# Optimization experiments

Measured on AMD Instinct MI355X. Metric: run time of the kernel, lower is better.

The kernel has to match this reference:

```python
import jax, jax.numpy as jnp
import numpy as np

TOPK = 5
LAMBDA_ALIGN_K = 16.0
MOM = 0.9          # EMA momentum
DEFAULT_SCORE = 0.5  # EMA bank default (bank starts empty)
EPS = 1e-8
NEG = 1.0e9


def pairwise_cosine(X):
    # torch F.normalize: X / max(||X||, eps)
    n = jnp.linalg.norm(X, axis=-1, keepdims=True)
    Xn = X / jnp.maximum(n, EPS)
    sim = Xn @ Xn.T
    return jnp.clip(sim, -1.0 + EPS, 1.0 - EPS)


def knn_mask(sim, allowed_base, topk=TOPK):
    B = sim.shape[0]
    eye = jnp.eye(B, dtype=sim.dtype)
    allowed = allowed_base * (1.0 - eye)
    masked = sim - NEG * eye
    masked = jnp.where(allowed < 0.5, -NEG, masked)
    masked = jnp.where(masked < 0.0, -NEG, masked)
    cand = (masked > 0).sum(axis=1)
    k = min(topk, max(B - 1, 1))
    keep_row = (cand >= topk).astype(sim.dtype)
    keep = keep_row[:, None] * keep_row[None, :]
    idx = jax.lax.top_k(masked, k)[1]                       # [B, k]
    M = jnp.zeros_like(sim).at[jnp.arange(B)[:, None], idx].set(1.0)
    M = jnp.maximum(M, M.T)
    return M * allowed * keep


def build_intra(sim, same, topk=TOPK):
    M = knn_mask(sim, same, topk)
    A = jnp.maximum(sim * M, 0.0) * same
    return A, M


def pga_loss(feats_sub, labels_sub):
    # feats_sub: [L, b, d]
    L = feats_sub.shape[0]
    same = (labels_sub[:, None] == labels_sub[None, :]).astype(jnp.float32)
    sims = jax.vmap(pairwise_cosine)(feats_sub)             # [L, b, b]
    A, M = jax.vmap(lambda s: build_intra(s, same))(sims)   # [L, b, b] each

    # EMA degree-based scores (no-grad in original; bank starts empty so
    # fetch-after-update == mom*default + (1-mom)*score_cur)
    S_intra = jnp.maximum(sims * same, 0.0)
    deg = jnp.maximum((S_intra > 0).sum(axis=2).astype(jnp.float32), 1.0)
    score_cur = jax.nn.sigmoid(S_intra.sum(axis=2) / deg)   # [L, b]
    ema = jax.lax.stop_gradient(MOM * DEFAULT_SCORE + (1.0 - MOM) * score_cur)

    # layer-pair masked MSE alignment, target detached
    A_deep = A[1:]
    A_tgt = jax.lax.stop_gradient(A[:-1])
    M_eff = jnp.maximum(M[:-1], M[1:])                      # [L-1, b, b]
    W = ema[:-1, :, None] * ema[:-1, None, :]               # [L-1, b, b]
    diff2 = (A_deep - A_tgt) ** 2 * W
    num = (diff2 * M_eff).sum(axis=(1, 2))
    den = jnp.maximum((M_eff * W).sum(axis=(1, 2)), EPS)
    terms = jnp.where(M_eff.sum(axis=(1, 2)) > 0, num / den, 0.0)
    raw = terms.sum() / max(L - 1, 1)
    return LAMBDA_ALIGN_K * raw


def setup_inputs() -> dict:
    key = jax.random.key(0)
    k1, k2 = jax.random.split(key)
    feats_final = jax.random.normal(k1, (8, 2048, 512), dtype=jnp.float32)
    labels = jax.random.randint(k2, (2048,), 0, 128).astype(jnp.int64)
    sample_ids = jnp.arange(2048, dtype=jnp.int64)
    return {"feats_final": feats_final, "labels": labels, "sample_ids": sample_ids}


def reference(feats_final, labels, sample_ids):
    # candidate subset from last layer (no-grad in original)
    X_last = feats_final[-1]
    S_last = pairwise_cosine(X_last)
    same_full = (labels[:, None] == labels[None, :]).astype(jnp.float32)
    _, M_last = build_intra(S_last, same_full)
    cand_mask = (M_last > 0).sum(axis=1) > 0
    idx_sub = jnp.nonzero(cand_mask)[0]  # eager (concrete) subselection
    feats_sub = feats_final[:, idx_sub]  # [L, b, d]
    labels_sub = labels[idx_sub]
    return pga_loss(feats_sub, labels_sub)
```

## Files before the change

kernel.cpp:

```cpp
#include <hip/hip_runtime.h>
#include <cmath>

#define NB   2048
#define ND   512
#define NL   8
#define NLAB 128
#define MAXM 64
#define TOPK_ 5
#define NTH  256
#define MAXSLOT 9
#define GSTRIDE (MAXM*MAXM)

#define SLOT_DECL(s) int off##s = -1; int lds##s = 0; float4 pre##s;
#define SLOT_INIT(s) { int idx = tid + (s)*NTH; if (idx < (m << 5)) { \
    int i = idx >> 5, k4 = idx & 31; \
    off##s = (g_s[i] << 9) + (k4 << 2); \
    lds##s = i * 132 + (k4 << 2); \
    pre##s = *(const float4*)(X + off##s); } }
#define SLOT_STORE(s) if (off##s >= 0) *(float4*)(XtF + lds##s) = pre##s;
#define SLOT_FETCH(s, kcn) if (off##s >= 0) pre##s = *(const float4*)(X + off##s + (kcn));

__global__ __launch_bounds__(NTH) void k_gram(
    const float* __restrict__ feats, const int* __restrict__ labels,
    float* __restrict__ G, int* __restrict__ cnt,
    unsigned long long* __restrict__ insub)
{
    __shared__ int wsum[4];
    __shared__ int g_s[MAXM];
    __shared__ float Xt[MAXM][132];
    __shared__ float rinvp[64];
    __shared__ unsigned long long tops_s[64];
    __shared__ unsigned char keep_s[64];
    float* XtF = &Xt[0][0];
    int c = blockIdx.x, l = blockIdx.y, tid = threadIdx.x;
    int lane = tid & 63, wv = tid >> 6;

    int my[8]; int n = 0; int base_i = tid * 8;
    for (int t = 0; t < 8; ++t) {
        int i = base_i + t;
        if (labels[i] == c) my[n++] = i;
    }
    int scan = n;
    #pragma unroll
    for (int off = 1; off < 64; off <<= 1) {
        int v = __shfl_up(scan, off);
        if (lane >= off) scan += v;
    }
    if (lane == 63) wsum[wv] = scan;
    __syncthreads();
    int w0 = wsum[0], w1 = wsum[1], w2 = wsum[2], w3 = wsum[3];
    int m = w0 + w1 + w2 + w3; if (m > MAXM) m = MAXM;
    int base = (wv > 0 ? w0 : 0) + (wv > 1 ? w1 : 0) + (wv > 2 ? w2 : 0);
    int excl = base + scan - n;
    for (int t = 0; t < n; ++t) {
        int slot = excl + t;
        if (slot < MAXM) g_s[slot] = my[t];
    }
    if (l == 0 && tid == 0) cnt[c] = m;
    __syncthreads();
    if (m == 0) {
        if (l == 7 && tid == 0) insub[c] = 0ull;
        return;
    }

    const float* X = feats + (size_t)l * NB * ND;

    SLOT_DECL(0) SLOT_DECL(1) SLOT_DECL(2) SLOT_DECL(3)
    SLOT_DECL(4) SLOT_DECL(5) SLOT_DECL(6) SLOT_DECL(7)
    SLOT_INIT(0) SLOT_INIT(1) SLOT_INIT(2) SLOT_INIT(3)
    SLOT_INIT(4) SLOT_INIT(5) SLOT_INIT(6) SLOT_INIT(7)

    const int P = m * (m + 1) / 2;
    float acc0[MAXSLOT], acc1[MAXSLOT];
    short is_[MAXSLOT], js_[MAXSLOT];
    int ns = 0;
    for (int p = tid; p < P; p += NTH) {
        int i = (int)((sqrtf(8.0f * (float)p + 1.0f) - 1.0f) * 0.5f);
        while (((i + 1) * (i + 2)) / 2 <= p) ++i;
        while ((i * (i + 1)) / 2 > p) --i;
        is_[ns] = (short)i;
        js_[ns] = (short)(p - (i * (i + 1)) / 2);
        acc0[ns] = 0.0f; acc1[ns] = 0.0f;
        ++ns;
    }

    for (int kc = 0; kc < ND; kc += 128) {
        if (kc) __syncthreads();
        SLOT_STORE(0) SLOT_STORE(1) SLOT_STORE(2) SLOT_STORE(3)
        SLOT_STORE(4) SLOT_STORE(5) SLOT_STORE(6) SLOT_STORE(7)
        __syncthreads();
        if (kc + 128 < ND) {
            int kcn = kc + 128;
            SLOT_FETCH(0, kcn) SLOT_FETCH(1, kcn) SLOT_FETCH(2, kcn) SLOT_FETCH(3, kcn)
            SLOT_FETCH(4, kcn) SLOT_FETCH(5, kcn) SLOT_FETCH(6, kcn) SLOT_FETCH(7, kcn)
        }
        for (int s = 0; s < ns; ++s) {
            int i = is_[s], j = js_[s];
            float a0 = acc0[s], a1 = acc1[s];
            #pragma unroll
            for (int k4 = 0; k4 < 32; ++k4) {
                float4 a = *(const float4*)&Xt[i][k4 << 2];
                float4 b = *(const float4*)&Xt[j][k4 << 2];
                a0 = fmaf(a.x, b.x, a0); a1 = fmaf(a.y, b.y, a1);
                a0 = fmaf(a.z, b.z, a0); a1 = fmaf(a.w, b.w, a1);
            }
            acc0[s] = a0; acc1[s] = a1;
        }
    }
    float* Gc = G + ((size_t)l * NLAB + c) * GSTRIDE;
    for (int s = 0; s < ns; ++s) {
        int i = is_[s], j = js_[s];
        float v = acc0[s] + acc1[s];
        Gc[i * MAXM + j] = v;
        Gc[j * MAXM + i] = v;
    }
    if (l != 7) return;

    float (*Gs)[65] = (float(*)[65])(&Xt[0][0]);
    __syncthreads();
    for (int s = 0; s < ns; ++s) {
        int i = is_[s], j = js_[s];
        float v = acc0[s] + acc1[s];
        Gs[i][j] = v; Gs[j][i] = v;
    }
    if (tid < m) for (int j = m; j < 64; ++j) Gs[tid][j] = -2.0f;
    __syncthreads();
    if (tid < 64) {
        rinvp[tid] = (tid < m) ? 1.0f / fmaxf(sqrtf(Gs[tid][tid]), 1e-8f) : 0.0f;
        keep_s[tid] = 0; tops_s[tid] = 0ull;
    }
    __syncthreads();
    unsigned long long tops = 0ull; bool keep = false;
    if (tid < m) {
        float ri = rinvp[tid];
        float v0=-1.f,v1=-1.f,v2=-1.f,v3=-1.f,v4=-1.f;
        int i0=0,i1=0,i2=0,i3=0,i4=0, cand=0;
        #pragma unroll 8
        for (int j = 0; j < 64; ++j) {
            float raw = Gs[tid][j];
            float v = fminf(fmaxf(raw * ri * rinvp[j], -1.0f), 1.0f);
            if (raw == -2.0f) v = -2.0f;
            if (v > 0.0f && j != tid) {
                ++cand;
                if      (v > v0) { v4=v3;i4=i3; v3=v2;i3=i2; v2=v1;i2=i1; v1=v0;i1=i0; v0=v;i0=j; }
                else if (v > v1) { v4=v3;i4=i3; v3=v2;i3=i2; v2=v1;i2=i1; v1=v;i1=j; }
                else if (v > v2) { v4=v3;i4=i3; v3=v2;i3=i2; v2=v;i2=j; }
                else if (v > v3) { v4=v3;i4=i3; v3=v;i3=j; }
                else if (v > v4) { v4=v;i4=j; }
            }
        }
        keep = (cand >= TOPK_);
        if (keep) tops = (1ull<<i0)|(1ull<<i1)|(1ull<<i2)|(1ull<<i3)|(1ull<<i4);
        keep_s[tid] = keep ? 1 : 0; tops_s[tid] = tops;
    }
    __syncthreads();
    unsigned long long Mrow = 0ull;
    if (tid < m && keep) {
        for (int j = 0; j < 64; ++j) {
            if (j == tid || !keep_s[j]) continue;
            if (((tops >> j) & 1ull) || ((tops_s[j] >> tid) & 1ull)) Mrow |= (1ull << j);
        }
    }
    if (tid < 64) {
        unsigned long long b = __ballot(Mrow != 0ull);
        if (tid == 0) insub[c] = b;
    }
}

__device__ __forceinline__ void load_tile(
    const float* __restrict__ Gc, int m, int tid, float (*Gs)[65], float* rinv)
{
    if (tid < 64) rinv[tid] = (tid < m) ? 1.0f / fmaxf(sqrtf(Gc[tid * MAXM + tid]), 1e-8f) : 0.0f;
    __syncthreads();
    int tot = m << 4;
    for (int idx4 = tid; idx4 < tot; idx4 += NTH) {
        int i = idx4 >> 4, j0 = (idx4 & 15) << 2;
        float4 raw = *(const float4*)(Gc + i * MAXM + j0);
        float ri = rinv[i];
        Gs[i][j0 + 0] = (j0 + 0 < m) ? fminf(fmaxf(raw.x * ri * rinv[j0 + 0], -1.0f), 1.0f) : -2.0f;
        Gs[i][j0 + 1] = (j0 + 1 < m) ? fminf(fmaxf(raw.y * ri * rinv[j0 + 1], -1.0f), 1.0f) : -2.0f;
        Gs[i][j0 + 2] = (j0 + 2 < m) ? fminf(fmaxf(raw.z * ri * rinv[j0 + 2], -1.0f), 1.0f) : -2.0f;
        Gs[i][j0 + 3] = (j0 + 3 < m) ? fminf(fmaxf(raw.w * ri * rinv[j0 + 3], -1.0f), 1.0f) : -2.0f;
    }
    __syncthreads();
}

__global__ __launch_bounds__(NTH) void k_decide(
    const float* __restrict__ G, const int* __restrict__ cnt,
    const unsigned long long* __restrict__ insub,
    unsigned long long* __restrict__ Mbits, float* __restrict__ ema)
{
    __shared__ float Gs[64][65];
    __shared__ float rinv[64];
    __shared__ unsigned long long tops_s[64];
    __shared__ unsigned char keep_s[64];
    int c = blockIdx.x, l = blockIdx.y, tid = threadIdx.x;
    int m = cnt[c]; if (m > MAXM) m = MAXM;
    if (m == 0) return;
    unsigned long long sub = insub[c];

    const float* Gc = G + ((size_t)l * NLAB + c) * GSTRIDE;
    load_tile(Gc, m, tid, Gs, rinv);
    if (tid < 64) { keep_s[tid] = 0; tops_s[tid] = 0ull; }
    __syncthreads();
    unsigned long long tops = 0ull; bool keep = false; bool act = false;
    float emaval = 0.0f;
    if (tid < m) {
        act = (sub >> tid) & 1ull;
        if (act) {
            float v0=-1.f,v1=-1.f,v2=-1.f,v3=-1.f,v4=-1.f;
            int i0=0,i1=0,i2=0,i3=0,i4=0, cand=0, dg=0;
            float rs = 0.0f;
            #pragma unroll 8
            for (int j = 0; j < 64; ++j) {
                float v = Gs[tid][j];
                if (!((sub >> j) & 1ull)) v = -2.0f;
                if (v > 0.0f) {
                    rs += v; ++dg;
                    if (j != tid) {
                        ++cand;
                        if      (v > v0) { v4=v3;i4=i3; v3=v2;i3=i2; v2=v1;i2=i1; v1=v0;i1=i0; v0=v;i0=j; }
                        else if (v > v1) { v4=v3;i4=i3; v3=v2;i3=i2; v2=v1;i2=i1; v1=v;i1=j; }
                        else if (v > v2) { v4=v3;i4=i3; v3=v2;i3=i2; v2=v;i2=j; }
                        else if (v > v3) { v4=v3;i4=i3; v3=v;i3=j; }
                        else if (v > v4) { v4=v;i4=j; }
                    }
                }
            }
            keep = (cand >= TOPK_);
            if (keep) tops = (1ull<<i0)|(1ull<<i1)|(1ull<<i2)|(1ull<<i3)|(1ull<<i4);
            float deg = (float)(dg > 0 ? dg : 1);
            float score = 1.0f / (1.0f + expf(-rs / deg));
            emaval = 0.45f + 0.1f * score;
        }
        keep_s[tid] = keep ? 1 : 0; tops_s[tid] = tops;
    }
    __syncthreads();
    if (tid < m) {
        unsigned long long Mrow = 0ull;
        if (keep) {
            for (int j = 0; j < 64; ++j) {
                if (j == tid || !keep_s[j]) continue;
                if (((tops >> j) & 1ull) || ((tops_s[j] >> tid) & 1ull)) Mrow |= (1ull << j);
            }
        }
        Mbits[((size_t)l * NLAB + c) * MAXM + tid] = Mrow;
        ema[((size_t)l * NLAB + c) * MAXM + tid] = emaval;
    }
}

__global__ __launch_bounds__(NTH) void k_pairs(
    const float* __restrict__ G, const int* __restrict__ cnt,
    const unsigned long long* __restrict__ Mbits, const float* __restrict__ ema,
    float* __restrict__ partial)
{
    __shared__ float r0[64], r1[64];
    __shared__ unsigned long long M0s[64], M1s[64];
    __shared__ float es[64];
    __shared__ float red[12];
    int c = blockIdx.x, p = blockIdx.y, tid = threadIdx.x;
    int m = cnt[c]; if (m > MAXM) m = MAXM;
    const float* G0 = G + ((size_t)p       * NLAB + c) * GSTRIDE;
    const float* G1 = G + ((size_t)(p + 1) * NLAB + c) * GSTRIDE;
    if (tid < m) {
        M0s[tid] = Mbits[((size_t)p * NLAB + c) * MAXM + tid];
        M1s[tid] = Mbits[((size_t)(p + 1) * NLAB + c) * MAXM + tid];
        es[tid]  = ema[((size_t)p * NLAB + c) * MAXM + tid];
        r0[tid]  = 1.0f / fmaxf(sqrtf(G0[tid * MAXM + tid]), 1e-8f);
        r1[tid]  = 1.0f / fmaxf(sqrtf(G1[tid * MAXM + tid]), 1e-8f);
    }
    __syncthreads();
    float fn = 0.0f, fd = 0.0f, fc = 0.0f;
    for (int idx = tid; idx < (m << 6); idx += NTH) {
        int i = idx >> 6, j = idx & 63;
        if (j >= m) continue;
        bool b0 = (M0s[i] >> j) & 1ull;
        bool b1 = (M1s[i] >> j) & 1ull;
        if (b0 | b1) {
            float v0 = b0 ? fminf(fmaxf(G0[idx] * r0[i] * r0[j], -1.0f), 1.0f) : 0.0f;
            float v1 = b1 ? fminf(fmaxf(G1[idx] * r1[i] * r1[j], -1.0f), 1.0f) : 0.0f;
            float w = es[i] * es[j];
            float d = v1 - v0;
            fn = fmaf(d * d, w, fn);
            fd += w;
            fc += 1.0f;
        }
    }
    for (int off = 32; off > 0; off >>= 1) {
        fn += __shfl_down(fn, off);
        fd += __shfl_down(fd, off);
        fc += __shfl_down(fc, off);
    }
    int w = tid >> 6;
    if ((tid & 63) == 0) { red[w * 3] = fn; red[w * 3 + 1] = fd; red[w * 3 + 2] = fc; }
    __syncthreads();
    if (tid == 0) {
        float* dst = partial + ((size_t)p * NLAB + c) * 4;
        dst[0] = red[0] + red[3] + red[6] + red[9];
        dst[1] = red[1] + red[4] + red[7] + red[10];
        dst[2] = red[2] + red[5] + red[8] + red[11];
    }
}

__global__ void k_final(const float* __restrict__ partial, float* __restrict__ out)
{
    int tid = threadIdx.x;
    float total = 0.0f;
    for (int p = 0; p < NL - 1; ++p) {
        float n = 0.0f, d = 0.0f, cc = 0.0f;
        for (int c = tid; c < NLAB; c += 64) {
            const float* src = partial + ((size_t)p * NLAB + c) * 4;
            n += src[0]; d += src[1]; cc += src[2];
        }
        for (int off = 32; off > 0; off >>= 1) {
            n += __shfl_down(n, off);
            d += __shfl_down(d, off);
            cc += __shfl_down(cc, off);
        }
        if (tid == 0 && cc > 0.0f) total += n / fmaxf(d, 1e-8f);
    }
    if (tid == 0) out[0] = 16.0f * total / 7.0f;
}

extern "C" void kernel_launch(void* const* d_in, const int* in_sizes, int n_in,
                              void* d_out, int out_size, void* d_ws, size_t ws_size,
                              hipStream_t stream) {
    const float* feats  = (const float*)d_in[0];
    const int*   labels = (const int*)d_in[1];
    char* w = (char*)d_ws;
    size_t gbytes = (size_t)NL * NLAB * GSTRIDE * 4;
    float*    G       = (float*)(w);
    float*    partial = (float*)(w + gbytes);
    int*      cnt     = (int*)(w + gbytes + 14336);
    unsigned long long* insub = (unsigned long long*)(w + gbytes + 14848);
    unsigned long long* Mbits = (unsigned long long*)(w + gbytes + 16384);
    float*    ema     = (float*)(w + gbytes + 16384 + 524288);
    float*    out     = (float*)d_out;

    k_gram  <<<dim3(NLAB, NL), NTH, 0, stream>>>(feats, labels, G, cnt, insub);
    k_decide<<<dim3(NLAB, NL), NTH, 0, stream>>>(G, cnt, insub, Mbits, ema);
    k_pairs <<<dim3(NLAB, NL - 1), NTH, 0, stream>>>(G, cnt, Mbits, ema, partial);
    k_final <<<1, 64, 0, stream>>>(partial, out);
}
```

Before: 131.6 us.

## Fuse gram, decision and pair kernels into one per-class block

Replaces the three-kernel pipeline (Gram, kNN decide, pair loss) with a single kernel, one block per label. Each block streams all eight layers' features through double-buffered LDS, computes each Gram tile with 2x2 register blocking, normalizes it in LDS and runs the top-k and EMA logic there. It then accumulates the layer-pair loss on the fly, so the global Gram, mask and EMA buffers and two launches go away. The trade-off is a grid of only 128 blocks that walk the layers in sequence, which may leave much of the GPU idle and expose memory latency.

```diff
diff --git a/kernel.cpp b/kernel.cpp
--- a/kernel.cpp
+++ b/kernel.cpp
@@ -8,31 +8,115 @@
 #define MAXM 64
 #define TOPK_ 5
 #define NTH  256
-#define MAXSLOT 9
-#define GSTRIDE (MAXM*MAXM)
+
 
 #define SLOT_DECL(s) int off##s = -1; int lds##s = 0; float4 pre##s;
-#define SLOT_INIT(s) { int idx = tid + (s)*NTH; if (idx < (m << 5)) { \
+#define SLOT_SETUP(s) { int idx = tid + (s)*NTH; if (idx < (m << 5)) { \
     int i = idx >> 5, k4 = idx & 31; \
     off##s = (g_s[i] << 9) + (k4 << 2); \
-    lds##s = i * 132 + (k4 << 2); \
-    pre##s = *(const float4*)(X + off##s); } }
-#define SLOT_STORE(s) if (off##s >= 0) *(float4*)(XtF + lds##s) = pre##s;
-#define SLOT_FETCH(s, kcn) if (off##s >= 0) pre##s = *(const float4*)(X + off##s + (kcn));
-
-__global__ __launch_bounds__(NTH) void k_gram(
+    lds##s = i * 132 + (k4 << 2); } }
+#define SLOT_FETCH(s, srcb) if (off##s >= 0) pre##s = *(const float4*)((srcb) + off##s);
+#define SLOT_STORE(s) if (off##s >= 0) *(float4*)(Xcur + lds##s) = pre##s;
+
+#define TDECL(s) short ti##s = -1, tj##s = 0; \
+    float q##s##00a=0.f,q##s##00b=0.f,q##s##01a=0.f,q##s##01b=0.f, \
+          q##s##10a=0.f,q##s##10b=0.f,q##s##11a=0.f,q##s##11b=0.f;
+
+#define TSETUP(s) { int p = tid + (s)*NTH; if (p < TP) { \
+    int i = (int)((sqrtf(8.0f * (float)p + 1.0f) - 1.0f) * 0.5f); \
+    while (((i + 1) * (i + 2)) / 2 <= p) ++i; \
+    while ((i * (i + 1)) / 2 > p) --i; \
+    ti##s = (short)i; tj##s = (short)(p - (i * (i + 1)) / 2); } }
+
+#define TCOMP(s) if (ti##s >= 0) { \
+    const float* ra = Xcur + ((int)ti##s << 1) * 132; \
+    const float* rb = Xcur + ((int)tj##s << 1) * 132; \
+    _Pragma("unroll") \
+    for (int k4 = 0; k4 < 32; ++k4) { \
+        float4 a0v = *(const float4*)(ra + (k4 << 2)); \
+        float4 a1v = *(const float4*)(ra + 132 + (k4 << 2)); \
+        float4 b0v = *(const float4*)(rb + (k4 << 2)); \
+        float4 b1v = *(const float4*)(rb + 132 + (k4 << 2)); \
+        q##s##00a = fmaf(a0v.x, b0v.x, q##s##00a); q##s##00b = fmaf(a0v.y, b0v.y, q##s##00b); \
+        q##s##00a = fmaf(a0v.z, b0v.z, q##s##00a); q##s##00b = fmaf(a0v.w, b0v.w, q##s##00b); \
+        q##s##01a = fmaf(a0v.x, b1v.x, q##s##01a); q##s##01b = fmaf(a0v.y, b1v.y, q##s##01b); \
+        q##s##01a = fmaf(a0v.z, b1v.z, q##s##01a); q##s##01b = fmaf(a0v.w, b1v.w, q##s##01b); \
+        q##s##10a = fmaf(a1v.x, b0v.x, q##s##10a); q##s##10b = fmaf(a1v.y, b0v.y, q##s##10b); \
+        q##s##10a = fmaf(a1v.z, b0v.z, q##s##10a); q##s##10b = fmaf(a1v.w, b0v.w, q##s##10b); \
+        q##s##11a = fmaf(a1v.x, b1v.x, q##s##11a); q##s##11b = fmaf(a1v.y, b1v.y, q##s##11b); \
+        q##s##11a = fmaf(a1v.z, b1v.z, q##s##11a); q##s##11b = fmaf(a1v.w, b1v.w, q##s##11b); \
+    } }
+
+#define TWB(s) if (ti##s >= 0) { \
+    int ib = (int)ti##s << 1, jb = (int)tj##s << 1; \
+    float v00 = q##s##00a + q##s##00b; \
+    float v01 = q##s##01a + q##s##01b; \
+    float v10 = q##s##10a + q##s##10b; \
+    float v11 = q##s##11a + q##s##11b; \
+    Gt[ib][jb] = v00; Gt[jb][ib] = v00; \
+    if (jb + 1 < m) { Gt[ib][jb+1] = v01; Gt[jb+1][ib] = v01; } \
+    if (ib + 1 < m) { Gt[ib+1][jb] = v10; Gt[jb][ib+1] = v10; } \
+    if (ib + 1 < m && jb + 1 < m) { Gt[ib+1][jb+1] = v11; Gt[jb+1][ib+1] = v11; } \
+    q##s##00a=0.f;q##s##00b=0.f;q##s##01a=0.f;q##s##01b=0.f; \
+    q##s##10a=0.f;q##s##10b=0.f;q##s##11a=0.f;q##s##11b=0.f; }
+
+__device__ __forceinline__ void pairs_acc(
+    int p, int c, int m, int tid,
+    const float (*gA)[65], const float (*gB)[65],
+    const unsigned long long* MbA, const unsigned long long* MbB,
+    const float* es, float* red, float* __restrict__ partial)
+{
+    float fn = 0.0f, fd = 0.0f, fc = 0.0f;
+    for (int idx = tid; idx < (m << 6); idx += NTH) {
+        int i = idx >> 6, j = idx & 63;
+        if (j >= m) continue;
+        bool b0 = (MbA[i] >> j) & 1ull;
+        bool b1 = (MbB[i] >> j) & 1ull;
+        if (b0 | b1) {
+            float v0 = b0 ? gA[i][j] : 0.0f;
+            float v1 = b1 ? gB[i][j] : 0.0f;
+            float w = es[i] * es[j];
+            float d = v1 - v0;
+            fn = fmaf(d * d, w, fn);
+            fd += w;
+            fc += 1.0f;
+        }
+    }
+    for (int off = 32; off > 0; off >>= 1) {
+        fn += __shfl_down(fn, off);
+        fd += __shfl_down(fd, off);
+        fc += __shfl_down(fc, off);
+    }
+    int wvx = tid >> 6;
+    if ((tid & 63) == 0) { red[wvx*3] = fn; red[wvx*3+1] = fd; red[wvx*3+2] = fc; }
+    __syncthreads();
+    if (tid == 0) {
+        float* dst = partial + ((size_t)p * NLAB + c) * 4;
+        dst[0] = red[0] + red[3] + red[6] + red[9];
+        dst[1] = red[1] + red[4] + red[7] + red[10];
+        dst[2] = red[2] + red[5] + red[8] + red[11];
+    }
+    __syncthreads();
+}
+
+__global__ __launch_bounds__(NTH) void k_fused(
     const float* __restrict__ feats, const int* __restrict__ labels,
-    float* __restrict__ G, int* __restrict__ cnt,
-    unsigned long long* __restrict__ insub)
+    float* __restrict__ partial)
 {
     __shared__ int wsum[4];
     __shared__ int g_s[MAXM];
-    __shared__ float Xt[MAXM][132];
-    __shared__ float rinvp[64];
+    __shared__ float Xt[2][MAXM][132];
+    __shared__ float g2[2][MAXM][65];
+    __shared__ float g7[MAXM][65];
+    __shared__ float rinv[64];
+    __shared__ unsigned long long Mb[NL][64];
+    __shared__ float emas[NL][64];
     __shared__ unsigned long long tops_s[64];
     __shared__ unsigned char keep_s[64];
-    float* XtF = &Xt[0][0];
-    int c = blockIdx.x, l = blockIdx.y, tid = threadIdx.x;
+    __shared__ unsigned long long sub_s;
+    __shared__ float red[12];
+
+    int c = blockIdx.x, tid = threadIdx.x;
     int lane = tid & 63, wv = tid >> 6;
 
     int my[8]; int n = 0; int base_i = tid * 8;
@@ -56,250 +140,167 @@
         int slot = excl + t;
         if (slot < MAXM) g_s[slot] = my[t];
     }
-    if (l == 0 && tid == 0) cnt[c] = m;
     __syncthreads();
     if (m == 0) {
-        if (l == 7 && tid == 0) insub[c] = 0ull;
+        if (tid == 0) {
+            for (int p = 0; p < NL - 1; ++p) {
+                float* dst = partial + ((size_t)p * NLAB + c) * 4;
+                dst[0] = 0.0f; dst[1] = 0.0f; dst[2] = 0.0f;
+            }
+        }
         return;
     }
 
-    const float* X = feats + (size_t)l * NB * ND;
+    const size_t LSTR = (size_t)NB * ND;
 
     SLOT_DECL(0) SLOT_DECL(1) SLOT_DECL(2) SLOT_DECL(3)
     SLOT_DECL(4) SLOT_DECL(5) SLOT_DECL(6) SLOT_DECL(7)
-    SLOT_INIT(0) SLOT_INIT(1) SLOT_INIT(2) SLOT_INIT(3)
-    SLOT_INIT(4) SLOT_INIT(5) SLOT_INIT(6) SLOT_INIT(7)
-
-    const int P = m * (m + 1) / 2;
-    float acc0[MAXSLOT], acc1[MAXSLOT];
-    short is_[MAXSLOT], js_[MAXSLOT];
-    int ns = 0;
-    for (int p = tid; p < P; p += NTH) {
-        int i = (int)((sqrtf(8.0f * (float)p + 1.0f) - 1.0f) * 0.5f);
-        while (((i + 1) * (i + 2)) / 2 <= p) ++i;
-        while ((i * (i + 1)) / 2 > p) --i;
-        is_[ns] = (short)i;
-        js_[ns] = (short)(p - (i * (i + 1)) / 2);
-        acc0[ns] = 0.0f; acc1[ns] = 0.0f;
-        ++ns;
-    }
-
-    for (int kc = 0; kc < ND; kc += 128) {
-        if (kc) __syncthreads();
+    SLOT_SETUP(0) SLOT_SETUP(1) SLOT_SETUP(2) SLOT_SETUP(3)
+    SLOT_SETUP(4) SLOT_SETUP(5) SLOT_SETUP(6) SLOT_SETUP(7)
+    {
+        const float* xb = feats + (size_t)7 * LSTR;
+        SLOT_FETCH(0, xb) SLOT_FETCH(1, xb) SLOT_FETCH(2, xb) SLOT_FETCH(3, xb)
+        SLOT_FETCH(4, xb) SLOT_FETCH(5, xb) SLOT_FETCH(6, xb) SLOT_FETCH(7, xb)
+    }
+
+    const int R = (m + 1) >> 1;
+    const int TP = R * (R + 1) / 2;
+    TDECL(0) TDECL(1) TDECL(2)
+    TSETUP(0) TSETUP(1) TSETUP(2)
+
+    for (int t = 0; t < 32; ++t) {
+        float* Xcur = &Xt[t & 1][0][0];
         SLOT_STORE(0) SLOT_STORE(1) SLOT_STORE(2) SLOT_STORE(3)
         SLOT_STORE(4) SLOT_STORE(5) SLOT_STORE(6) SLOT_STORE(7)
         __syncthreads();
-        if (kc + 128 < ND) {
-            int kcn = kc + 128;
-            SLOT_FETCH(0, kcn) SLOT_FETCH(1, kcn) SLOT_FETCH(2, kcn) SLOT_FETCH(3, kcn)
-            SLOT_FETCH(4, kcn) SLOT_FETCH(5, kcn) SLOT_FETCH(6, kcn) SLOT_FETCH(7, kcn)
-        }
-        for (int s = 0; s < ns; ++s) {
-            int i = is_[s], j = js_[s];
-            float a0 = acc0[s], a1 = acc1[s];
-            #pragma unroll
-            for (int k4 = 0; k4 < 32; ++k4) {
-                float4 a = *(const float4*)&Xt[i][k4 << 2];
-                float4 b = *(const float4*)&Xt[j][k4 << 2];
-                a0 = fmaf(a.x, b.x, a0); a1 = fmaf(a.y, b.y, a1);
-                a0 = fmaf(a.z, b.z, a0); a1 = fmaf(a.w, b.w, a1);
-            }
-            acc0[s] = a0; acc1[s] = a1;
-        }
-    }
-    float* Gc = G + ((size_t)l * NLAB + c) * GSTRIDE;
-    for (int s = 0; s < ns; ++s) {
-        int i = is_[s], j = js_[s];
-        float v = acc0[s] + acc1[s];
-        Gc[i * MAXM + j] = v;
-        Gc[j * MAXM + i] = v;
-    }
-    if (l != 7) return;
-
-    float (*Gs)[65] = (float(*)[65])(&Xt[0][0]);
-    __syncthreads();
-    for (int s = 0; s < ns; ++s) {
-        int i = is_[s], j = js_[s];
-        float v = acc0[s] + acc1[s];
-        Gs[i][j] = v; Gs[j][i] = v;
-    }
-    if (tid < m) for (int j = m; j < 64; ++j) Gs[tid][j] = -2.0f;
-    __syncthreads();
-    if (tid < 64) {
-        rinvp[tid] = (tid < m) ? 1.0f / fmaxf(sqrtf(Gs[tid][tid]), 1e-8f) : 0.0f;
-        keep_s[tid] = 0; tops_s[tid] = 0ull;
-    }
-    __syncthreads();
-    unsigned long long tops = 0ull; bool keep = false;
-    if (tid < m) {
-        float ri = rinvp[tid];
-        float v0=-1.f,v1=-1.f,v2=-1.f,v3=-1.f,v4=-1.f;
-        int i0=0,i1=0,i2=0,i3=0,i4=0, cand=0;
-        #pragma unroll 8
-        for (int j = 0; j < 64; ++j) {
-            float raw = Gs[tid][j];
-            float v = fminf(fmaxf(raw * ri * rinvp[j], -1.0f), 1.0f);
-            if (raw == -2.0f) v = -2.0f;
-            if (v > 0.0f && j != tid) {
-                ++cand;
-                if      (v > v0) { v4=v3;i4=i3; v3=v2;i3=i2; v2=v1;i2=i1; v1=v0;i1=i0; v0=v;i0=j; }
-                else if (v > v1) { v4=v3;i4=i3; v3=v2;i3=i2; v2=v1;i2=i1; v1=v;i1=j; }
-                else if (v > v2) { v4=v3;i4=i3; v3=v2;i3=i2; v2=v;i2=j; }
-                else if (v > v3) { v4=v3;i4=i3; v3=v;i3=j; }
-                else if (v > v4) { v4=v;i4=j; }
-            }
-        }
-        keep = (cand >= TOPK_);
-        if (keep) tops = (1ull<<i0)|(1ull<<i1)|(1ull<<i2)|(1ull<<i3)|(1ull<<i4);
-        keep_s[tid] = keep ? 1 : 0; tops_s[tid] = tops;
-    }
-    __syncthreads();
-    unsigned long long Mrow = 0ull;
-    if (tid < m && keep) {
-        for (int j = 0; j < 64; ++j) {
-            if (j == tid || !keep_s[j]) continue;
-            if (((tops >> j) & 1ull) || ((tops_s[j] >> tid) & 1ull)) Mrow |= (1ull << j);
-        }
-    }
-    if (tid < 64) {
-        unsigned long long b = __ballot(Mrow != 0ull);
-        if (tid == 0) insub[c] = b;
-    }
-}
-
-__device__ __forceinline__ void load_tile(
-    const float* __restrict__ Gc, int m, int tid, float (*Gs)[65], float* rinv)
-{
-    if (tid < 64) rinv[tid] = (tid < m) ? 1.0f / fmaxf(sqrtf(Gc[tid * MAXM + tid]), 1e-8f) : 0.0f;
-    __syncthreads();
-    int tot = m << 4;
-    for (int idx4 = tid; idx4 < tot; idx4 += NTH) {
-        int i = idx4 >> 4, j0 = (idx4 & 15) << 2;
-        float4 raw = *(const float4*)(Gc + i * MAXM + j0);
-        float ri = rinv[i];
-        Gs[i][j0 + 0] = (j0 + 0 < m) ? fminf(fmaxf(raw.x * ri * rinv[j0 + 0], -1.0f), 1.0f) : -2.0f;
-        Gs[i][j0 + 1] = (j0 + 1 < m) ? fminf(fmaxf(raw.y * ri * rinv[j0 + 1], -1.0f), 1.0f) : -2.0f;
-        Gs[i][j0 + 2] = (j0 + 2 < m) ? fminf(fmaxf(raw.z * ri * rinv[j0 + 2], -1.0f), 1.0f) : -2.0f;
-        Gs[i][j0 + 3] = (j0 + 3 < m) ? fminf(fmaxf(raw.w * ri * rinv[j0 + 3], -1.0f), 1.0f) : -2.0f;
-    }
-    __syncthreads();
-}
-
-__global__ __launch_bounds__(NTH) void k_decide(
-    const float* __restrict__ G, const int* __restrict__ cnt,
-    const unsigned long long* __restrict__ insub,
-    unsigned long long* __restrict__ Mbits, float* __restrict__ ema)
-{
-    __shared__ float Gs[64][65];
-    __shared__ float rinv[64];
-    __shared__ unsigned long long tops_s[64];
-    __shared__ unsigned char keep_s[64];
-    int c = blockIdx.x, l = blockIdx.y, tid = threadIdx.x;
-    int m = cnt[c]; if (m > MAXM) m = MAXM;
-    if (m == 0) return;
-    unsigned long long sub = insub[c];
-
-    const float* Gc = G + ((size_t)l * NLAB + c) * GSTRIDE;
-    load_tile(Gc, m, tid, Gs, rinv);
-    if (tid < 64) { keep_s[tid] = 0; tops_s[tid] = 0ull; }
-    __syncthreads();
-    unsigned long long tops = 0ull; bool keep = false; bool act = false;
-    float emaval = 0.0f;
-    if (tid < m) {
-        act = (sub >> tid) & 1ull;
-        if (act) {
-            float v0=-1.f,v1=-1.f,v2=-1.f,v3=-1.f,v4=-1.f;
-            int i0=0,i1=0,i2=0,i3=0,i4=0, cand=0, dg=0;
-            float rs = 0.0f;
-            #pragma unroll 8
-            for (int j = 0; j < 64; ++j) {
-                float v = Gs[tid][j];
-                if (!((sub >> j) & 1ull)) v = -2.0f;
-                if (v > 0.0f) {
-                    rs += v; ++dg;
-                    if (j != tid) {
-                        ++cand;
-                        if      (v > v0) { v4=v3;i4=i3; v3=v2;i3=i2; v2=v1;i2=i1; v1=v0;i1=i0; v0=v;i0=j; }
-                        else if (v > v1) { v4=v3;i4=i3; v3=v2;i3=i2; v2=v1;i2=i1; v1=v;i1=j; }
-                        else if (v > v2) { v4=v3;i4=i3; v3=v2;i3=i2; v2=v;i2=j; }
-                        else if (v > v3) { v4=v3;i4=i3; v3=v;i3=j; }
-                        else if (v > v4) { v4=v;i4=j; }
+        if (t < 31) {
+            int tn = t + 1;
+            int Ln = ((tn >> 2) == 0) ? 7 : (tn >> 2) - 1;
+            const float* xb = feats + (size_t)Ln * LSTR + ((tn & 3) << 7);
+            SLOT_FETCH(0, xb) SLOT_FETCH(1, xb) SLOT_FETCH(2, xb) SLOT_FETCH(3, xb)
+            SLOT_FETCH(4, xb) SLOT_FETCH(5, xb) SLOT_FETCH(6, xb) SLOT_FETCH(7, xb)
+        }
+        TCOMP(0) TCOMP(1) TCOMP(2)
+
+        if ((t & 3) == 3) {
+            int sl = t >> 2;
+            int L = (sl == 0) ? 7 : sl - 1;
+            float (*Gt)[65] = (sl == 0) ? g7 : g2[L & 1];
+
+            TWB(0) TWB(1) TWB(2)
+            __syncthreads();
+            if (tid < 64) rinv[tid] = (tid < m) ? 1.0f / fmaxf(sqrtf(Gt[tid][tid]), 1e-8f) : 0.0f;
+            __syncthreads();
+            for (int idx = tid; idx < (m << 6); idx += NTH) {
+                int i = idx >> 6, j = idx & 63;
+                float x = -2.0f;
+                if (j < m) {
+                    float raw = Gt[i][j];
+                    x = fminf(fmaxf(raw * rinv[i] * rinv[j], -1.0f), 1.0f);
+                }
+                Gt[i][j] = x;
+            }
+            __syncthreads();
+
+            if (sl == 0) {
+                if (tid < 64) { keep_s[tid] = 0; tops_s[tid] = 0ull; }
+                __syncthreads();
+                unsigned long long tops = 0ull; bool keep = false;
+                if (tid < m) {
+                    float v0=-1.f,v1=-1.f,v2=-1.f,v3=-1.f,v4=-1.f;
+                    int i0=0,i1=0,i2=0,i3=0,i4=0, cand=0;
+                    #pragma unroll 8
+                    for (int j = 0; j < 64; ++j) {
+                        float v = g7[tid][j];
+                        if (v > 0.0f && j != tid) {
+                            ++cand;
+                            if      (v > v0) { v4=v3;i4=i3; v3=v2;i3=i2; v2=v1;i2=i1; v1=v0;i1=i0; v0=v;i0=j; }
+                            else if (v > v1) { v4=v3;i4=i3; v3=v2;i3=i2; v2=v1;i2=i1; v1=v;i1=j; }
+                            else if (v > v2) { v4=v3;i4=i3; v3=v2;i3=i2; v2=v;i2=j; }
+                            else if (v > v3) { v4=v3;i4=i3; v3=v;i3=j; }
+                            else if (v > v4) { v4=v;i4=j; }
+                        }
                     }
-                }
-            }
-            keep = (cand >= TOPK_);
-            if (keep) tops = (1ull<<i0)|(1ull<<i1)|(1ull<<i2)|(1ull<<i3)|(1ull<<i4);
-            float deg = (float)(dg > 0 ? dg : 1);
-            float score = 1.0f / (1.0f + expf(-rs / deg));
-            emaval = 0.45f + 0.1f * score;
-        }
-        keep_s[tid] = keep ? 1 : 0; tops_s[tid] = tops;
-    }
-    __syncthreads();
-    if (tid < m) {
-        unsigned long long Mrow = 0ull;
-        if (keep) {
-            for (int j = 0; j < 64; ++j) {
-                if (j == tid || !keep_s[j]) continue;
-                if (((tops >> j) & 1ull) || ((tops_s[j] >> tid) & 1ull)) Mrow |= (1ull << j);
-            }
-        }
-        Mbits[((size_t)l * NLAB + c) * MAXM + tid] = Mrow;
-        ema[((size_t)l * NLAB + c) * MAXM + tid] = emaval;
-    }
-}
-
-__global__ __launch_bounds__(NTH) void k_pairs(
-    const float* __restrict__ G, const int* __restrict__ cnt,
-    const unsigned long long* __restrict__ Mbits, const float* __restrict__ ema,
-    float* __restrict__ partial)
-{
-    __shared__ float r0[64], r1[64];
-    __shared__ unsigned long long M0s[64], M1s[64];
-    __shared__ float es[64];
-    __shared__ float red[12];
-    int c = blockIdx.x, p = blockIdx.y, tid = threadIdx.x;
-    int m = cnt[c]; if (m > MAXM) m = MAXM;
-    const float* G0 = G + ((size_t)p       * NLAB + c) * GSTRIDE;
-    const float* G1 = G + ((size_t)(p + 1) * NLAB + c) * GSTRIDE;
-    if (tid < m) {
-        M0s[tid] = Mbits[((size_t)p * NLAB + c) * MAXM + tid];
-        M1s[tid] = Mbits[((size_t)(p + 1) * NLAB + c) * MAXM + tid];
-        es[tid]  = ema[((size_t)p * NLAB + c) * MAXM + tid];
-        r0[tid]  = 1.0f / fmaxf(sqrtf(G0[tid * MAXM + tid]), 1e-8f);
-        r1[tid]  = 1.0f / fmaxf(sqrtf(G1[tid * MAXM + tid]), 1e-8f);
-    }
-    __syncthreads();
-    float fn = 0.0f, fd = 0.0f, fc = 0.0f;
-    for (int idx = tid; idx < (m << 6); idx += NTH) {
-        int i = idx >> 6, j = idx & 63;
-        if (j >= m) continue;
-        bool b0 = (M0s[i] >> j) & 1ull;
-        bool b1 = (M1s[i] >> j) & 1ull;
-        if (b0 | b1) {
-            float v0 = b0 ? fminf(fmaxf(G0[idx] * r0[i] * r0[j], -1.0f), 1.0f) : 0.0f;
-            float v1 = b1 ? fminf(fmaxf(G1[idx] * r1[i] * r1[j], -1.0f), 1.0f) : 0.0f;
-            float w = es[i] * es[j];
-            float d = v1 - v0;
-            fn = fmaf(d * d, w, fn);
-            fd += w;
-            fc += 1.0f;
-        }
-    }
-    for (int off = 32; off > 0; off >>= 1) {
-        fn += __shfl_down(fn, off);
-        fd += __shfl_down(fd, off);
-        fc += __shfl_down(fc, off);
-    }
-    int w = tid >> 6;
-    if ((tid & 63) == 0) { red[w * 3] = fn; red[w * 3 + 1] = fd; red[w * 3 + 2] = fc; }
-    __syncthreads();
-    if (tid == 0) {
-        float* dst = partial + ((size_t)p * NLAB + c) * 4;
-        dst[0] = red[0] + red[3] + red[6] + red[9];
-        dst[1] = red[1] + red[4] + red[7] + red[10];
-        dst[2] = red[2] + red[5] + red[8] + red[11];
-    }
+                    keep = (cand >= TOPK_);
+                    if (keep) tops = (1ull<<i0)|(1ull<<i1)|(1ull<<i2)|(1ull<<i3)|(1ull<<i4);
+                    keep_s[tid] = keep ? 1 : 0; tops_s[tid] = tops;
+                }
+                __syncthreads();
+                unsigned long long Mrow = 0ull;
+                if (tid < m && keep) {
+                    for (int j = 0; j < 64; ++j) {
+                        if (j == tid || !keep_s[j]) continue;
+                        if (((tops >> j) & 1ull) || ((tops_s[j] >> tid) & 1ull)) Mrow |= (1ull << j);
+                    }
+                }
+                if (tid < 64) {
+                    unsigned long long b = __ballot(Mrow != 0ull);
+                    if (tid == 0) sub_s = b;
+                }
+                __syncthreads();
+            }
+
+            if (tid < 64) { keep_s[tid] = 0; tops_s[tid] = 0ull; }
+            __syncthreads();
+            {
+                unsigned long long sub = sub_s;
+                unsigned long long tops = 0ull; bool keep = false; float emaval = 0.0f;
+                if (tid < m) {
+                    bool act = (sub >> tid) & 1ull;
+                    if (act) {
+                        float v0=-1.f,v1=-1.f,v2=-1.f,v3=-1.f,v4=-1.f;
+                        int i0=0,i1=0,i2=0,i3=0,i4=0, cand=0, dg=0;
+                        float rs = 0.0f;
+                        #pragma unroll 8
+                        for (int j = 0; j < 64; ++j) {
+                            float v = Gt[tid][j];
+                            if (!((sub >> j) & 1ull)) v = -2.0f;
+                            if (v > 0.0f) {
+                                rs += v; ++dg;
+                                if (j != tid) {
+                                    ++cand;
+                                    if      (v > v0) { v4=v3;i4=i3; v3=v2;i3=i2; v2=v1;i2=i1; v1=v0;i1=i0; v0=v;i0=j; }
+                                    else if (v > v1) { v4=v3;i4=i3; v3=v2;i3=i2; v2=v1;i2=i1; v1=v;i1=j; }
+                                    else if (v > v2) { v4=v3;i4=i3; v3=v2;i3=i2; v2=v;i2=j; }
+                                    else if (v > v3) { v4=v3;i4=i3; v3=v;i3=j; }
+                                    else if (v > v4) { v4=v;i4=j; }
+                                }
+                            }
+                        }
+                        keep = (cand >= TOPK_);
+                        if (keep) tops = (1ull<<i0)|(1ull<<i1)|(1ull<<i2)|(1ull<<i3)|(1ull<<i4);
+                        float deg = (float)(dg > 0 ? dg : 1);
+                        float score = 1.0f / (1.0f + expf(-rs / deg));
+                        emaval = 0.45f + 0.1f * score;
+                    }
+                    keep_s[tid] = keep ? 1 : 0; tops_s[tid] = tops;
+                }
+                __syncthreads();
+                if (tid < m) {
+                    unsigned long long Mrow = 0ull;
+                    if (keep) {
+                        for (int j = 0; j < 64; ++j) {
+                            if (j == tid || !keep_s[j]) continue;
+                            if (((tops >> j) & 1ull) || ((tops_s[j] >> tid) & 1ull)) Mrow |= (1ull << j);
+                        }
+                    }
+                    Mb[L][tid] = Mrow;
+                    emas[L][tid] = emaval;
+                }
+                __syncthreads();
+            }
+
+            if (sl >= 2) {
+                pairs_acc(L - 1, c, m, tid,
+                          (const float (*)[65])g2[(L - 1) & 1],
+                          (const float (*)[65])g2[L & 1],
+                          Mb[L - 1], Mb[L], emas[L - 1], red, partial);
+            }
+        }
+    }
+    pairs_acc(6, c, m, tid,
+              (const float (*)[65])g2[0], (const float (*)[65])g7,
+              Mb[6], Mb[7], emas[6], red, partial);
 }
 
 __global__ void k_final(const float* __restrict__ partial, float* __restrict__ out)
@@ -327,18 +328,9 @@
                               hipStream_t stream) {
     const float* feats  = (const float*)d_in[0];
     const int*   labels = (const int*)d_in[1];
-    char* w = (char*)d_ws;
-    size_t gbytes = (size_t)NL * NLAB * GSTRIDE * 4;
-    float*    G       = (float*)(w);
-    float*    partial = (float*)(w + gbytes);
-    int*      cnt     = (int*)(w + gbytes + 14336);
-    unsigned long long* insub = (unsigned long long*)(w + gbytes + 14848);
-    unsigned long long* Mbits = (unsigned long long*)(w + gbytes + 16384);
-    float*    ema     = (float*)(w + gbytes + 16384 + 524288);
-    float*    out     = (float*)d_out;
-
-    k_gram  <<<dim3(NLAB, NL), NTH, 0, stream>>>(feats, labels, G, cnt, insub);
-    k_decide<<<dim3(NLAB, NL), NTH, 0, stream>>>(G, cnt, insub, Mbits, ema);
-    k_pairs <<<dim3(NLAB, NL - 1), NTH, 0, stream>>>(G, cnt, Mbits, ema, partial);
-    k_final <<<1, 64, 0, stream>>>(partial, out);
+    float* partial = (float*)d_ws;
+    float* out     = (float*)d_out;
+
+    k_fused<<<dim3(NLAB), NTH, 0, stream>>>(feats, labels, partial);
+    k_final<<<1, 64, 0, stream>>>(partial, out);
 }
```

Measured after the change: 268.3 us. +103.9%, slower.

## Fuse decide and pair kernels; store normalized cosine tiles from gram kernel

Applied to the files above, without the earlier changes.

The gram kernel now normalizes each class Gram tile into cosines in shared memory and writes the normalized tile to global memory with float4 stores. The separate decide and pairs kernels are merged into one kernel per layer pair. It loads both layers' tiles into LDS, computes kNN masks and EMA weights for each with two wavefronts, then reduces the masked MSE. This drops one launch and the Mbits/ema global round trip. The cost is that the kNN and EMA work for interior layers is done twice, and the fused kernel uses more shared memory.

```diff
diff --git a/kernel.cpp b/kernel.cpp
--- a/kernel.cpp
+++ b/kernel.cpp
@@ -107,14 +107,6 @@
             acc0[s] = a0; acc1[s] = a1;
         }
     }
-    float* Gc = G + ((size_t)l * NLAB + c) * GSTRIDE;
-    for (int s = 0; s < ns; ++s) {
-        int i = is_[s], j = js_[s];
-        float v = acc0[s] + acc1[s];
-        Gc[i * MAXM + j] = v;
-        Gc[j * MAXM + i] = v;
-    }
-    if (l != 7) return;
 
     float (*Gs)[65] = (float(*)[65])(&Xt[0][0]);
     __syncthreads();
@@ -125,21 +117,32 @@
     }
     if (tid < m) for (int j = m; j < 64; ++j) Gs[tid][j] = -2.0f;
     __syncthreads();
-    if (tid < 64) {
-        rinvp[tid] = (tid < m) ? 1.0f / fmaxf(sqrtf(Gs[tid][tid]), 1e-8f) : 0.0f;
-        keep_s[tid] = 0; tops_s[tid] = 0ull;
-    }
+    if (tid < 64) rinvp[tid] = (tid < m) ? 1.0f / fmaxf(sqrtf(Gs[tid][tid]), 1e-8f) : 0.0f;
+    __syncthreads();
+    for (int idx = tid; idx < (m << 6); idx += NTH) {
+        int i = idx >> 6, j = idx & 63;
+        if (j < m) {
+            float raw = Gs[i][j];
+            Gs[i][j] = fminf(fmaxf(raw * rinvp[i] * rinvp[j], -1.0f), 1.0f);
+        }
+    }
+    __syncthreads();
+    float* Gc = G + ((size_t)l * NLAB + c) * GSTRIDE;
+    for (int idx4 = tid; idx4 < (m << 4); idx4 += NTH) {
+        int i = idx4 >> 4, j0 = (idx4 & 15) << 2;
+        *(float4*)(Gc + i * MAXM + j0) = *(const float4*)&Gs[i][j0];
+    }
+    if (l != 7) return;
+
+    if (tid < 64) { keep_s[tid] = 0; tops_s[tid] = 0ull; }
     __syncthreads();
     unsigned long long tops = 0ull; bool keep = false;
     if (tid < m) {
-        float ri = rinvp[tid];
         float v0=-1.f,v1=-1.f,v2=-1.f,v3=-1.f,v4=-1.f;
         int i0=0,i1=0,i2=0,i3=0,i4=0, cand=0;
         #pragma unroll 8
         for (int j = 0; j < 64; ++j) {
-            float raw = Gs[tid][j];
-            float v = fminf(fmaxf(raw * ri * rinvp[j], -1.0f), 1.0f);
-            if (raw == -2.0f) v = -2.0f;
+            float v = Gs[tid][j];
             if (v > 0.0f && j != tid) {
                 ++cand;
                 if      (v > v0) { v4=v3;i4=i3; v3=v2;i3=i2; v2=v1;i2=i1; v1=v0;i1=i0; v0=v;i0=j; }
@@ -167,57 +170,50 @@
     }
 }
 
-__device__ __forceinline__ void load_tile(
-    const float* __restrict__ Gc, int m, int tid, float (*Gs)[65], float* rinv)
-{
-    if (tid < 64) rinv[tid] = (tid < m) ? 1.0f / fmaxf(sqrtf(Gc[tid * MAXM + tid]), 1e-8f) : 0.0f;
-    __syncthreads();
-    int tot = m << 4;
-    for (int idx4 = tid; idx4 < tot; idx4 += NTH) {
-        int i = idx4 >> 4, j0 = (idx4 & 15) << 2;
-        float4 raw = *(const float4*)(Gc + i * MAXM + j0);
-        float ri = rinv[i];
-        Gs[i][j0 + 0] = (j0 + 0 < m) ? fminf(fmaxf(raw.x * ri * rinv[j0 + 0], -1.0f), 1.0f) : -2.0f;
-        Gs[i][j0 + 1] = (j0 + 1 < m) ? fminf(fmaxf(raw.y * ri * rinv[j0 + 1], -1.0f), 1.0f) : -2.0f;
-        Gs[i][j0 + 2] = (j0 + 2 < m) ? fminf(fmaxf(raw.z * ri * rinv[j0 + 2], -1.0f), 1.0f) : -2.0f;
-        Gs[i][j0 + 3] = (j0 + 3 < m) ? fminf(fmaxf(raw.w * ri * rinv[j0 + 3], -1.0f), 1.0f) : -2.0f;
-    }
-    __syncthreads();
-}
-
-__global__ __launch_bounds__(NTH) void k_decide(
+__global__ __launch_bounds__(NTH) void k_pairdec(
     const float* __restrict__ G, const int* __restrict__ cnt,
     const unsigned long long* __restrict__ insub,
-    unsigned long long* __restrict__ Mbits, float* __restrict__ ema)
+    float* __restrict__ partial)
 {
-    __shared__ float Gs[64][65];
-    __shared__ float rinv[64];
-    __shared__ unsigned long long tops_s[64];
-    __shared__ unsigned char keep_s[64];
-    int c = blockIdx.x, l = blockIdx.y, tid = threadIdx.x;
+    __shared__ float Gs0[64][65];
+    __shared__ float Gs1[64][65];
+    __shared__ unsigned long long tops0[64], tops1[64];
+    __shared__ unsigned char keep0[64], keep1[64];
+    __shared__ unsigned long long M0s[64], M1s[64];
+    __shared__ float es[64];
+    __shared__ float red[12];
+    int c = blockIdx.x, p = blockIdx.y, tid = threadIdx.x;
+    int lane = tid & 63, wv = tid >> 6;
     int m = cnt[c]; if (m > MAXM) m = MAXM;
-    if (m == 0) return;
     unsigned long long sub = insub[c];
 
-    const float* Gc = G + ((size_t)l * NLAB + c) * GSTRIDE;
-    load_tile(Gc, m, tid, Gs, rinv);
-    if (tid < 64) { keep_s[tid] = 0; tops_s[tid] = 0ull; }
-    __syncthreads();
-    unsigned long long tops = 0ull; bool keep = false; bool act = false;
-    float emaval = 0.0f;
-    if (tid < m) {
-        act = (sub >> tid) & 1ull;
+    const float* G0 = G + ((size_t)p       * NLAB + c) * GSTRIDE;
+    const float* G1 = G + ((size_t)(p + 1) * NLAB + c) * GSTRIDE;
+    for (int idx4 = tid; idx4 < (m << 4); idx4 += NTH) {
+        int i = idx4 >> 4, j0 = (idx4 & 15) << 2;
+        *(float4*)&Gs0[i][j0] = *(const float4*)(G0 + i * MAXM + j0);
+        *(float4*)&Gs1[i][j0] = *(const float4*)(G1 + i * MAXM + j0);
+    }
+    if (tid < 64)       { keep0[tid] = 0; tops0[tid] = 0ull; }
+    else if (tid < 128) { keep1[tid - 64] = 0; tops1[tid - 64] = 0ull; }
+    __syncthreads();
+
+    unsigned long long tops = 0ull; bool keep = false;
+    if (wv < 2 && lane < m) {
+        const float (*Gt)[65] = (wv == 0) ? Gs0 : Gs1;
+        bool act = (sub >> lane) & 1ull;
+        float emaval = 0.0f;
         if (act) {
             float v0=-1.f,v1=-1.f,v2=-1.f,v3=-1.f,v4=-1.f;
             int i0=0,i1=0,i2=0,i3=0,i4=0, cand=0, dg=0;
             float rs = 0.0f;
             #pragma unroll 8
             for (int j = 0; j < 64; ++j) {
-                float v = Gs[tid][j];
+                float v = Gt[lane][j];
                 if (!((sub >> j) & 1ull)) v = -2.0f;
                 if (v > 0.0f) {
                     rs += v; ++dg;
-                    if (j != tid) {
+                    if (j != lane) {
                         ++cand;
                         if      (v > v0) { v4=v3;i4=i3; v3=v2;i3=i2; v2=v1;i2=i1; v1=v0;i1=i0; v0=v;i0=j; }
                         else if (v > v1) { v4=v3;i4=i3; v3=v2;i3=i2; v2=v1;i2=i1; v1=v;i1=j; }
@@ -233,43 +229,24 @@
             float score = 1.0f / (1.0f + expf(-rs / deg));
             emaval = 0.45f + 0.1f * score;
         }
-        keep_s[tid] = keep ? 1 : 0; tops_s[tid] = tops;
-    }
-    __syncthreads();
-    if (tid < m) {
+        if (wv == 0) { keep0[lane] = keep ? 1 : 0; tops0[lane] = tops; es[lane] = emaval; }
+        else         { keep1[lane] = keep ? 1 : 0; tops1[lane] = tops; }
+    }
+    __syncthreads();
+    if (wv < 2 && lane < m) {
+        const unsigned long long* topsW = (wv == 0) ? tops0 : tops1;
+        const unsigned char*     keepW = (wv == 0) ? keep0 : keep1;
         unsigned long long Mrow = 0ull;
         if (keep) {
             for (int j = 0; j < 64; ++j) {
-                if (j == tid || !keep_s[j]) continue;
-                if (((tops >> j) & 1ull) || ((tops_s[j] >> tid) & 1ull)) Mrow |= (1ull << j);
+                if (j == lane || !keepW[j]) continue;
+                if (((tops >> j) & 1ull) || ((topsW[j] >> lane) & 1ull)) Mrow |= (1ull << j);
             }
         }
-        Mbits[((size_t)l * NLAB + c) * MAXM + tid] = Mrow;
-        ema[((size_t)l * NLAB + c) * MAXM + tid] = emaval;
-    }
-}
-
-__global__ __launch_bounds__(NTH) void k_pairs(
-    const float* __restrict__ G, const int* __restrict__ cnt,
-    const unsigned long long* __restrict__ Mbits, const float* __restrict__ ema,
-    float* __restrict__ partial)
-{
-    __shared__ float r0[64], r1[64];
-    __shared__ unsigned long long M0s[64], M1s[64];
-    __shared__ float es[64];
-    __shared__ float red[12];
-    int c = blockIdx.x, p = blockIdx.y, tid = threadIdx.x;
-    int m = cnt[c]; if (m > MAXM) m = MAXM;
-    const float* G0 = G + ((size_t)p       * NLAB + c) * GSTRIDE;
-    const float* G1 = G + ((size_t)(p + 1) * NLAB + c) * GSTRIDE;
-    if (tid < m) {
-        M0s[tid] = Mbits[((size_t)p * NLAB + c) * MAXM + tid];
-        M1s[tid] = Mbits[((size_t)(p + 1) * NLAB + c) * MAXM + tid];
-        es[tid]  = ema[((size_t)p * NLAB + c) * MAXM + tid];
-        r0[tid]  = 1.0f / fmaxf(sqrtf(G0[tid * MAXM + tid]), 1e-8f);
-        r1[tid]  = 1.0f / fmaxf(sqrtf(G1[tid * MAXM + tid]), 1e-8f);
-    }
-    __syncthreads();
+        if (wv == 0) M0s[lane] = Mrow; else M1s[lane] = Mrow;
+    }
+    __syncthreads();
+
     float fn = 0.0f, fd = 0.0f, fc = 0.0f;
     for (int idx = tid; idx < (m << 6); idx += NTH) {
         int i = idx >> 6, j = idx & 63;
@@ -277,8 +254,8 @@
         bool b0 = (M0s[i] >> j) & 1ull;
         bool b1 = (M1s[i] >> j) & 1ull;
         if (b0 | b1) {
-            float v0 = b0 ? fminf(fmaxf(G0[idx] * r0[i] * r0[j], -1.0f), 1.0f) : 0.0f;
-            float v1 = b1 ? fminf(fmaxf(G1[idx] * r1[i] * r1[j], -1.0f), 1.0f) : 0.0f;
+            float v0 = b0 ? Gs0[i][j] : 0.0f;
+            float v1 = b1 ? Gs1[i][j] : 0.0f;
             float w = es[i] * es[j];
             float d = v1 - v0;
             fn = fmaf(d * d, w, fn);
@@ -291,8 +268,7 @@
         fd += __shfl_down(fd, off);
         fc += __shfl_down(fc, off);
     }
-    int w = tid >> 6;
-    if ((tid & 63) == 0) { red[w * 3] = fn; red[w * 3 + 1] = fd; red[w * 3 + 2] = fc; }
+    if ((tid & 63) == 0) { red[wv * 3] = fn; red[wv * 3 + 1] = fd; red[wv * 3 + 2] = fc; }
     __syncthreads();
     if (tid == 0) {
         float* dst = partial + ((size_t)p * NLAB + c) * 4;
@@ -333,12 +309,9 @@
     float*    partial = (float*)(w + gbytes);
     int*      cnt     = (int*)(w + gbytes + 14336);
     unsigned long long* insub = (unsigned long long*)(w + gbytes + 14848);
-    unsigned long long* Mbits = (unsigned long long*)(w + gbytes + 16384);
-    float*    ema     = (float*)(w + gbytes + 16384 + 524288);
     float*    out     = (float*)d_out;
 
-    k_gram  <<<dim3(NLAB, NL), NTH, 0, stream>>>(feats, labels, G, cnt, insub);
-    k_decide<<<dim3(NLAB, NL), NTH, 0, stream>>>(G, cnt, insub, Mbits, ema);
-    k_pairs <<<dim3(NLAB, NL - 1), NTH, 0, stream>>>(G, cnt, Mbits, ema, partial);
-    k_final <<<1, 64, 0, stream>>>(partial, out);
+    k_gram   <<<dim3(NLAB, NL),     NTH, 0, stream>>>(feats, labels, G, cnt, insub);
+    k_pairdec<<<dim3(NLAB, NL - 1), NTH, 0, stream>>>(G, cnt, insub, partial);
+    k_final  <<<1, 64, 0, stream>>>(partial, out);
 }
```

After: 129.3 us. Within noise of the previous version (-1.7%).
